# Kernel tuning notes

Hardware: AMD Instinct MI355X
Metric: run time of the kernel (lower is better)

Reference implementation:

```python
import jax, jax.numpy as jnp
import numpy as np

N = 100000          # nodes
E = 1600000         # edges (before self-loops)
F_IN = 128          # dataset.num_node_features
HID = 32            # hidden_channels
HEADS = 4
NUM_CLASSES = 40
NEG_SLOPE = 0.2     # PyG GATConv default


def setup_inputs() -> dict:
    key = jax.random.key(0)
    ks = jax.random.split(key, 16)
    x = jax.random.normal(ks[0], (N, F_IN), dtype=jnp.float32)
    edge_index = jax.random.randint(ks[1], (2, E), 0, N, dtype=jnp.int64)

    def glorot(k, shape):
        lim = float(np.sqrt(6.0 / (shape[0] + shape[-1])))
        return jax.random.uniform(k, shape, jnp.float32, -lim, lim)

    # layer 0: F_IN -> HID, heads=HEADS, concat
    W0 = glorot(ks[2], (F_IN, HEADS * HID))
    as0 = glorot(ks[3], (HEADS, HID))
    ad0 = glorot(ks[4], (HEADS, HID))
    b0 = jnp.zeros((HEADS * HID,), jnp.float32)
    # layer 1: HEADS*HID -> HID, heads=HEADS, concat
    W1 = glorot(ks[5], (HEADS * HID, HEADS * HID))
    as1 = glorot(ks[6], (HEADS, HID))
    ad1 = glorot(ks[7], (HEADS, HID))
    b1 = jnp.zeros((HEADS * HID,), jnp.float32)
    # layer 2: HEADS*HID -> HID, heads=1, no concat
    W2 = glorot(ks[8], (HEADS * HID, HID))
    as2 = glorot(ks[9], (1, HID))
    ad2 = glorot(ks[10], (1, HID))
    b2 = jnp.zeros((HID,), jnp.float32)
    # final linear HID -> NUM_CLASSES
    lin_w = glorot(ks[11], (HID, NUM_CLASSES))
    lin_b = jnp.zeros((NUM_CLASSES,), jnp.float32)
    return dict(x=x, edge_index=edge_index, W0=W0, as0=as0, ad0=ad0, b0=b0,
                W1=W1, as1=as1, ad1=ad1, b1=b1,
                W2=W2, as2=as2, ad2=ad2, b2=b2, lin_w=lin_w, lin_b=lin_b)


def gat_conv(x, src, dst, W, a_src, a_dst, b, heads, out_ch, concat):
    n = x.shape[0]
    h = (x @ W).reshape(n, heads, out_ch)               # [N,H,C]
    alpha_s = (h * a_src).sum(-1)                        # [N,H]
    alpha_d = (h * a_dst).sum(-1)                        # [N,H]
    e = jax.nn.leaky_relu(alpha_s[src] + alpha_d[dst], NEG_SLOPE)  # [E,H]
    m = jax.ops.segment_max(e, dst, num_segments=n)      # segment softmax over in-edges
    e = jnp.exp(e - m[dst])
    denom = jax.ops.segment_sum(e, dst, num_segments=n)
    alpha = e / (denom[dst] + 1e-16)                     # [E,H]
    out = jax.ops.segment_sum(h[src] * alpha[:, :, None], dst, num_segments=n)  # [N,H,C]
    out = out.reshape(n, heads * out_ch) if concat else out.mean(axis=1)
    return out + b


def reference(x, edge_index, W0, as0, ad0, b0, W1, as1, ad1, b1,
              W2, as2, ad2, b2, lin_w, lin_b):
    n = x.shape[0]
    loop = jnp.arange(n, dtype=edge_index.dtype)
    src = jnp.concatenate([edge_index[0], loop])   # PyG GATConv adds self-loops
    dst = jnp.concatenate([edge_index[1], loop])
    x = jax.nn.relu(gat_conv(x, src, dst, W0, as0, ad0, b0, HEADS, HID, True))
    x = jax.nn.relu(gat_conv(x, src, dst, W1, as1, ad1, b1, HEADS, HID, True))
    x = jax.nn.relu(gat_conv(x, src, dst, W2, as2, ad2, b2, 1, HID, False))
    return x @ lin_w + lin_b
```

## Files before the change

kernel.cpp:

```cpp
#include <hip/hip_runtime.h>
#include <hip/hip_bf16.h>
#include <hip/hip_fp16.h>
#include <math.h>


#define NEG_SLOPE 0.2f


__global__ void zero1_kernel(int* __restrict__ a, int n) {
    int i = blockIdx.x * blockDim.x + threadIdx.x;
    if (i < n) a[i] = 0;
}

__global__ void count_rank_kernel(const int* __restrict__ ei, int eraw, int n,
                                  int* __restrict__ deg, int* __restrict__ rank) {
    int i = blockIdx.x * blockDim.x + threadIdx.x;
    int etot = eraw + n;
    if (i >= etot) return;
    int dst = (i < eraw) ? ei[eraw + i] : (i - eraw);
    rank[i] = atomicAdd(&deg[dst], 1);
}

__global__ __launch_bounds__(1024)
void scan_local_kernel(const int* __restrict__ deg, int* __restrict__ rowptr,
                       int* __restrict__ bsum, int n) {
    __shared__ int buf[1024];
    int tid = threadIdx.x;
    int i = blockIdx.x * 1024 + tid;
    int v = (i < n) ? deg[i] : 0;
    buf[tid] = v;
    __syncthreads();
    for (int off = 1; off < 1024; off <<= 1) {
        int t = (tid >= off) ? buf[tid - off] : 0;
        __syncthreads();
        buf[tid] += t;
        __syncthreads();
    }
    if (i < n) rowptr[i] = buf[tid] - v;
    if (tid == 1023) bsum[blockIdx.x] = buf[1023];
}

__global__ __launch_bounds__(128)
void scan_sums_kernel(const int* __restrict__ bsum, int* __restrict__ boffs, int nb) {
    __shared__ int buf[128];
    int tid = threadIdx.x;
    int v = (tid < nb) ? bsum[tid] : 0;
    buf[tid] = v;
    __syncthreads();
    for (int off = 1; off < 128; off <<= 1) {
        int t = (tid >= off) ? buf[tid - off] : 0;
        __syncthreads();
        buf[tid] += t;
        __syncthreads();
    }
    if (tid < nb) boffs[tid] = buf[tid] - v;
}

__global__ void scan_add_kernel(int* __restrict__ rowptr, const int* __restrict__ boffs,
                                int n, int etot) {
    int i = blockIdx.x * blockDim.x + threadIdx.x;
    if (i < n) rowptr[i] += boffs[i >> 10];
    if (i == 0) rowptr[n] = etot;
}

__global__ void scatter2_kernel(const int* __restrict__ ei, const int* __restrict__ rank,
                                int eraw, int n, const int* __restrict__ rowptr,
                                int* __restrict__ csr_src) {
    int i = blockIdx.x * blockDim.x + threadIdx.x;
    int etot = eraw + n;
    if (i >= etot) return;
    int src, dst;
    if (i < eraw) { src = ei[i]; dst = ei[eraw + i]; }
    else          { src = i - eraw; dst = src; }
    csr_src[rowptr[dst] + rank[i]] = src;
}


struct h4pack { __half2 a, b; };

__global__ __launch_bounds__(256)
void gemm_rt_f32in_kernel(const float* __restrict__ X, const float* __restrict__ W,
                          __half* __restrict__ H, int n) {
    __shared__ float xsT[128][36];
    int t = threadIdx.x;
    int base = blockIdx.x * 32;
    {
        int r  = t >> 3;
        int k0 = (t & 7) << 4;
        const float4* xp = (const float4*)(X + (size_t)(base + r) * 128 + k0);
        float4 a = xp[0], b = xp[1], c = xp[2], d = xp[3];
        xsT[k0 +  0][r] = a.x; xsT[k0 +  1][r] = a.y; xsT[k0 +  2][r] = a.z; xsT[k0 +  3][r] = a.w;
        xsT[k0 +  4][r] = b.x; xsT[k0 +  5][r] = b.y; xsT[k0 +  6][r] = b.z; xsT[k0 +  7][r] = b.w;
        xsT[k0 +  8][r] = c.x; xsT[k0 +  9][r] = c.y; xsT[k0 + 10][r] = c.z; xsT[k0 + 11][r] = c.w;
        xsT[k0 + 12][r] = d.x; xsT[k0 + 13][r] = d.y; xsT[k0 + 14][r] = d.z; xsT[k0 + 15][r] = d.w;
    }
    __syncthreads();

    int tx = t & 31;
    int ty = t >> 5;
    float4 acc0 = make_float4(0.f, 0.f, 0.f, 0.f);
    float4 acc1 = acc0, acc2 = acc0, acc3 = acc0;
    const float4* W4 = (const float4*)W;

#pragma unroll 4
    for (int k = 0; k < 128; k++) {
        float4 w  = W4[k * 32 + tx];
        float4 xv = *(const float4*)(&xsT[k][ty << 2]);
        acc0.x += xv.x * w.x; acc0.y += xv.x * w.y; acc0.z += xv.x * w.z; acc0.w += xv.x * w.w;
        acc1.x += xv.y * w.x; acc1.y += xv.y * w.y; acc1.z += xv.y * w.z; acc1.w += xv.y * w.w;
        acc2.x += xv.z * w.x; acc2.y += xv.z * w.y; acc2.z += xv.z * w.z; acc2.w += xv.z * w.w;
        acc3.x += xv.w * w.x; acc3.y += xv.w * w.y; acc3.z += xv.w * w.z; acc3.w += xv.w * w.w;
    }

    size_t row0 = (size_t)(base + (ty << 2));
    h4pack* hp = (h4pack*)(H + row0 * 128) + tx;
    h4pack p;
    p.a = __floats2half2_rn(acc0.x, acc0.y); p.b = __floats2half2_rn(acc0.z, acc0.w);
    hp[0]  = p;
    p.a = __floats2half2_rn(acc1.x, acc1.y); p.b = __floats2half2_rn(acc1.z, acc1.w);
    hp[32] = p;
    p.a = __floats2half2_rn(acc2.x, acc2.y); p.b = __floats2half2_rn(acc2.z, acc2.w);
    hp[64] = p;
    p.a = __floats2half2_rn(acc3.x, acc3.y); p.b = __floats2half2_rn(acc3.z, acc3.w);
    hp[96] = p;
}

__global__ __launch_bounds__(256)
void gemm_rt_f16in_kernel(const __half* __restrict__ X, const float* __restrict__ W,
                          __half* __restrict__ H, int n) {
    __shared__ float xsT[128][36];
    int t = threadIdx.x;
    int base = blockIdx.x * 32;
    {
        int r  = t >> 3;
        int k0 = (t & 7) << 4;
        const uint4* xp = (const uint4*)(X + (size_t)(base + r) * 128 + k0);
        uint4 a = xp[0], b = xp[1];
        float2 f;
        f = __half22float2(*(const __half2*)&a.x); xsT[k0 +  0][r] = f.x; xsT[k0 +  1][r] = f.y;
        f = __half22float2(*(const __half2*)&a.y); xsT[k0 +  2][r] = f.x; xsT[k0 +  3][r] = f.y;
        f = __half22float2(*(const __half2*)&a.z); xsT[k0 +  4][r] = f.x; xsT[k0 +  5][r] = f.y;
        f = __half22float2(*(const __half2*)&a.w); xsT[k0 +  6][r] = f.x; xsT[k0 +  7][r] = f.y;
        f = __half22float2(*(const __half2*)&b.x); xsT[k0 +  8][r] = f.x; xsT[k0 +  9][r] = f.y;
        f = __half22float2(*(const __half2*)&b.y); xsT[k0 + 10][r] = f.x; xsT[k0 + 11][r] = f.y;
        f = __half22float2(*(const __half2*)&b.z); xsT[k0 + 12][r] = f.x; xsT[k0 + 13][r] = f.y;
        f = __half22float2(*(const __half2*)&b.w); xsT[k0 + 14][r] = f.x; xsT[k0 + 15][r] = f.y;
    }
    __syncthreads();

    int tx = t & 31;
    int ty = t >> 5;
    float4 acc0 = make_float4(0.f, 0.f, 0.f, 0.f);
    float4 acc1 = acc0, acc2 = acc0, acc3 = acc0;
    const float4* W4 = (const float4*)W;

#pragma unroll 4
    for (int k = 0; k < 128; k++) {
        float4 w  = W4[k * 32 + tx];
        float4 xv = *(const float4*)(&xsT[k][ty << 2]);
        acc0.x += xv.x * w.x; acc0.y += xv.x * w.y; acc0.z += xv.x * w.z; acc0.w += xv.x * w.w;
        acc1.x += xv.y * w.x; acc1.y += xv.y * w.y; acc1.z += xv.y * w.z; acc1.w += xv.y * w.w;
        acc2.x += xv.z * w.x; acc2.y += xv.z * w.y; acc2.z += xv.z * w.z; acc2.w += xv.z * w.w;
        acc3.x += xv.w * w.x; acc3.y += xv.w * w.y; acc3.z += xv.w * w.z; acc3.w += xv.w * w.w;
    }

    size_t row0 = (size_t)(base + (ty << 2));
    h4pack* hp = (h4pack*)(H + row0 * 128) + tx;
    h4pack p;
    p.a = __floats2half2_rn(acc0.x, acc0.y); p.b = __floats2half2_rn(acc0.z, acc0.w);
    hp[0]  = p;
    p.a = __floats2half2_rn(acc1.x, acc1.y); p.b = __floats2half2_rn(acc1.z, acc1.w);
    hp[32] = p;
    p.a = __floats2half2_rn(acc2.x, acc2.y); p.b = __floats2half2_rn(acc2.z, acc2.w);
    hp[64] = p;
    p.a = __floats2half2_rn(acc3.x, acc3.y); p.b = __floats2half2_rn(acc3.z, acc3.w);
    hp[96] = p;
}


__global__ __launch_bounds__(128)
void gemm_l2_f16_kernel(const __half* __restrict__ X, const float* __restrict__ W,
                        __half* __restrict__ H, int n) {
    __shared__ float xs[8][129];
    int base = blockIdx.x * 8;
    int tid = threadIdx.x;
#pragma unroll
    for (int it = 0; it < 4; it++) {
        int i = tid + it * 128;
        int r = i >> 6, c2 = i & 63;
        int row = base + r;
        __half2 v = (row < n) ? ((const __half2*)(X + (size_t)row * 128))[c2]
                              : __floats2half2_rn(0.f, 0.f);
        float2 f = __half22float2(v);
        xs[r][c2 * 2] = f.x; xs[r][c2 * 2 + 1] = f.y;
    }
    __syncthreads();
    int col  = tid & 31;
    int rsub = tid >> 5;
    float acc0 = 0.f, acc1 = 0.f;
    for (int k = 0; k < 128; k++) {
        float w = W[k * 32 + col];
        acc0 += xs[rsub][k] * w;
        acc1 += xs[rsub + 4][k] * w;
    }
    int row0 = base + rsub;
    if (row0 < n)     H[(size_t)row0 * 32 + col]       = __float2half(acc0);
    if (row0 + 4 < n) H[(size_t)(row0 + 4) * 32 + col] = __float2half(acc1);
}


__global__ void attn_coef_f16_kernel(const __half* __restrict__ H,
                                     const float* __restrict__ a_s,
                                     const float* __restrict__ a_d,
                                     float* __restrict__ as_out,
                                     float* __restrict__ ad_out, int n) {
    int i = blockIdx.x * blockDim.x + threadIdx.x;
    if (i >= n * 4) return;
    int node = i >> 2, h = i & 3;
    const __half2* hp = (const __half2*)(H + (size_t)node * 128 + h * 32);
    float s = 0.f, d = 0.f;
#pragma unroll
    for (int c2 = 0; c2 < 16; c2++) {
        float2 v = __half22float2(hp[c2]);
        s += v.x * a_s[h * 32 + c2 * 2] + v.y * a_s[h * 32 + c2 * 2 + 1];
        d += v.x * a_d[h * 32 + c2 * 2] + v.y * a_d[h * 32 + c2 * 2 + 1];
    }
    as_out[i] = s;
    ad_out[i] = d;
}

__global__ void attn_coef_l2_f16_kernel(const __half* __restrict__ H,
                                        const float* __restrict__ a_s,
                                        const float* __restrict__ a_d,
                                        float* __restrict__ as_out,
                                        float* __restrict__ ad_out, int n) {
    int i = blockIdx.x * blockDim.x + threadIdx.x;
    if (i >= n) return;
    const __half2* hp = (const __half2*)(H + (size_t)i * 32);
    float s = 0.f, d = 0.f;
#pragma unroll
    for (int c2 = 0; c2 < 16; c2++) {
        float2 v = __half22float2(hp[c2]);
        s += v.x * a_s[2 * c2] + v.y * a_s[2 * c2 + 1];
        d += v.x * a_d[2 * c2] + v.y * a_d[2 * c2 + 1];
    }
    as_out[i] = s;
    ad_out[i] = d;
}


__global__ __launch_bounds__(256)
void gat_fused_f16_kernel(const __half* __restrict__ Hm,
                          const float* __restrict__ as_,
                          const float* __restrict__ ad_,
                          const int* __restrict__ rowptr,
                          const int* __restrict__ csr,
                          const float* __restrict__ bias,
                          __half* __restrict__ out, int n) {
    constexpr int GS = 32;
    int t = threadIdx.x;
    int node = blockIdx.x * 8 + (t >> 5);
    if (node >= n) return;
    int tl = t & 31;
    int h  = tl >> 3;
    int k8 = tl & 7;
    const uint2* H8 = (const uint2*)Hm;
    int e0 = rowptr[node], e1 = rowptr[node + 1];
    float ad_d = ad_[(size_t)node * 4 + h];

    int  ce  = e0 + k8;
    bool vA  = ce < e1;
    int  idxA = vA ? csr[ce] : 0;
    float asA = vA ? as_[(size_t)idxA * 4 + h] : 0.f;

    float m = -INFINITY, l = 0.f;
    float4 acc = make_float4(0.f, 0.f, 0.f, 0.f);

    for (int eb = e0; eb < e1; eb += 8) {
        uint2 u[8];
#pragma unroll
        for (int j = 0; j < 8; j++) {
            int src = __shfl(idxA, j, 8);
            u[j] = H8[(size_t)src * GS + tl];
        }

        int  ne  = eb + 8 + k8;
        bool vB  = ne < e1;
        int  idxB = vB ? csr[ne] : 0;
        float asB = vB ? as_[(size_t)idxB * 4 + h] : 0.f;

        float el = asA + ad_d;
        el = (el > 0.f) ? el : NEG_SLOPE * el;
        el = vA ? el : -INFINITY;

        float cm = el;
        cm = fmaxf(cm, __shfl_xor(cm, 1, 8));
        cm = fmaxf(cm, __shfl_xor(cm, 2, 8));
        cm = fmaxf(cm, __shfl_xor(cm, 4, 8));
        float m_new = fmaxf(m, cm);
        float scale = __expf(m - m_new);
        float p = vA ? __expf(el - m_new) : 0.f;

        float ps = p;
        ps += __shfl_xor(ps, 1, 8);
        ps += __shfl_xor(ps, 2, 8);
        ps += __shfl_xor(ps, 4, 8);
        l = l * scale + ps;
        acc.x *= scale; acc.y *= scale; acc.z *= scale; acc.w *= scale;
        m = m_new;

#pragma unroll
        for (int j = 0; j < 8; j++) {
            float pj  = __shfl(p, j, 8);
            float2 f01 = __half22float2(*(const __half2*)&u[j].x);
            float2 f23 = __half22float2(*(const __half2*)&u[j].y);
            acc.x += pj * f01.x; acc.y += pj * f01.y;
            acc.z += pj * f23.x; acc.w += pj * f23.y;
        }
        idxA = idxB; asA = asB; vA = vB;
    }

    float li = 1.f / (l + 1e-16f);
    float4 b4 = ((const float4*)bias)[tl];
    float4 o;
    o.x = fmaxf(acc.x * li + b4.x, 0.f);
    o.y = fmaxf(acc.y * li + b4.y, 0.f);
    o.z = fmaxf(acc.z * li + b4.z, 0.f);
    o.w = fmaxf(acc.w * li + b4.w, 0.f);
    h4pack po;
    po.a = __floats2half2_rn(o.x, o.y);
    po.b = __floats2half2_rn(o.z, o.w);
    ((h4pack*)out)[(size_t)node * 32 + tl] = po;
}


__global__ __launch_bounds__(256)
void gat_fused_l2_kernel(const __half* __restrict__ Hm,
                         const float* __restrict__ as_,
                         const float* __restrict__ ad_,
                         const int* __restrict__ rowptr,
                         const int* __restrict__ csr,
                         const float* __restrict__ bias,
                         const float* __restrict__ lw,
                         const float* __restrict__ lb,
                         float* __restrict__ out, int n) {
    int t = threadIdx.x;
    int node = blockIdx.x * 32 + (t >> 3);
    if (node >= n) return;
    int tl = t & 7;
    const uint2* H8 = (const uint2*)Hm;
    int e0 = rowptr[node], e1 = rowptr[node + 1];
    float ad_d = ad_[node];

    int  ce  = e0 + tl;
    bool vA  = ce < e1;
    int  idxA = vA ? csr[ce] : 0;
    float asA = vA ? as_[idxA] : 0.f;

    float m = -INFINITY, l = 0.f;
    float4 acc = make_float4(0.f, 0.f, 0.f, 0.f);

    for (int eb = e0; eb < e1; eb += 8) {
        uint2 u[8];
#pragma unroll
        for (int j = 0; j < 8; j++) {
            int src = __shfl(idxA, j, 8);
            u[j] = H8[(size_t)src * 8 + tl];
        }

        int  ne  = eb + 8 + tl;
        bool vB  = ne < e1;
        int  idxB = vB ? csr[ne] : 0;
        float asB = vB ? as_[idxB] : 0.f;

        float el = asA + ad_d;
        el = (el > 0.f) ? el : NEG_SLOPE * el;
        el = vA ? el : -INFINITY;

        float cm = el;
        cm = fmaxf(cm, __shfl_xor(cm, 1, 8));
        cm = fmaxf(cm, __shfl_xor(cm, 2, 8));
        cm = fmaxf(cm, __shfl_xor(cm, 4, 8));
        float m_new = fmaxf(m, cm);
        float scale = __expf(m - m_new);
        float p = vA ? __expf(el - m_new) : 0.f;

        float ps = p;
        ps += __shfl_xor(ps, 1, 8);
        ps += __shfl_xor(ps, 2, 8);
        ps += __shfl_xor(ps, 4, 8);
        l = l * scale + ps;
        acc.x *= scale; acc.y *= scale; acc.z *= scale; acc.w *= scale;
        m = m_new;

#pragma unroll
        for (int j = 0; j < 8; j++) {
            float pj  = __shfl(p, j, 8);
            float2 f01 = __half22float2(*(const __half2*)&u[j].x);
            float2 f23 = __half22float2(*(const __half2*)&u[j].y);
            acc.x += pj * f01.x; acc.y += pj * f01.y;
            acc.z += pj * f23.x; acc.w += pj * f23.y;
        }
        idxA = idxB; asA = asB; vA = vB;
    }

    float li = 1.f / (l + 1e-16f);
    float4 b4 = ((const float4*)bias)[tl];
    float4 o;
    o.x = fmaxf(acc.x * li + b4.x, 0.f);
    o.y = fmaxf(acc.y * li + b4.y, 0.f);
    o.z = fmaxf(acc.z * li + b4.z, 0.f);
    o.w = fmaxf(acc.w * li + b4.w, 0.f);

    float fin0 = lb[tl];
    float fin1 = lb[tl + 8];
    float fin2 = lb[tl + 16];
    float fin3 = lb[tl + 24];
    float fin4 = lb[tl + 32];
#pragma unroll
    for (int j = 0; j < 8; j++) {
        float vx = __shfl(o.x, j, 8);
        float vy = __shfl(o.y, j, 8);
        float vz = __shfl(o.z, j, 8);
        float vw = __shfl(o.w, j, 8);
        const float* l0 = lw + (size_t)(4 * j) * 40;
#pragma unroll
        for (int c = 0; c < 5; c++) {
            int cls = tl + 8 * c;
            float v = vx * l0[cls] + vy * l0[40 + cls] + vz * l0[80 + cls] + vw * l0[120 + cls];
            if (c == 0) fin0 += v;
            else if (c == 1) fin1 += v;
            else if (c == 2) fin2 += v;
            else if (c == 3) fin3 += v;
            else fin4 += v;
        }
    }
    float* op = out + (size_t)node * 40;
    op[tl]      = fin0;
    op[tl + 8]  = fin1;
    op[tl + 16] = fin2;
    op[tl + 24] = fin3;
    op[tl + 32] = fin4;
}


extern "C" void kernel_launch(void* const* d_in, const int* in_sizes, int n_in,
                              void* d_out, int out_size, void* d_ws, size_t ws_size,
                              hipStream_t stream) {
    const float* x   = (const float*)d_in[0];
    const int*   ei  = (const int*)d_in[1];
    const float* W0  = (const float*)d_in[2];
    const float* as0 = (const float*)d_in[3];
    const float* ad0 = (const float*)d_in[4];
    const float* b0  = (const float*)d_in[5];
    const float* W1  = (const float*)d_in[6];
    const float* as1 = (const float*)d_in[7];
    const float* ad1 = (const float*)d_in[8];
    const float* b1  = (const float*)d_in[9];
    const float* W2  = (const float*)d_in[10];
    const float* as2 = (const float*)d_in[11];
    const float* ad2 = (const float*)d_in[12];
    const float* b2  = (const float*)d_in[13];
    const float* lw  = (const float*)d_in[14];
    const float* lb  = (const float*)d_in[15];
    float* out = (float*)d_out;

    const int n    = in_sizes[0] / 128;
    const int eraw = in_sizes[1] / 2;
    const int etot = eraw + n;
    const int nb   = (n + 1023) / 1024;

    char* wsp = (char*)d_ws;
    size_t off = 0;
    auto alloc = [&](size_t bytes) -> void* {
        void* p = wsp + off;
        off += (bytes + 255) & ~(size_t)255;
        return p;
    };
    __half* h16    = (__half*)alloc((size_t)n * 128 * 2);
    __half* buf16  = (__half*)alloc((size_t)n * 128 * 2);
    __half* h2     = (__half*)alloc((size_t)n * 32 * 2);
    float*  asb    = (float*)alloc((size_t)n * 4 * 4);
    float*  adb    = (float*)alloc((size_t)n * 4 * 4);
    int*    deg    = (int*)alloc((size_t)n * 4);
    int*    rank   = (int*)alloc((size_t)etot * 4);
    int*    rowptr = (int*)alloc((size_t)(n + 1) * 4);
    int*    csr    = (int*)alloc((size_t)etot * 4);
    int*    bsum   = (int*)alloc((size_t)nb * 4);
    int*    boffs  = (int*)alloc((size_t)nb * 4);

    zero1_kernel<<<(n + 255) / 256, 256, 0, stream>>>(deg, n);
    count_rank_kernel<<<(etot + 255) / 256, 256, 0, stream>>>(ei, eraw, n, deg, rank);
    scan_local_kernel<<<nb, 1024, 0, stream>>>(deg, rowptr, bsum, n);
    scan_sums_kernel<<<1, 128, 0, stream>>>(bsum, boffs, nb);
    scan_add_kernel<<<(n + 255) / 256, 256, 0, stream>>>(rowptr, boffs, n, etot);
    scatter2_kernel<<<(etot + 255) / 256, 256, 0, stream>>>(ei, rank, eraw, n, rowptr, csr);

    gemm_rt_f32in_kernel<<<n / 32, 256, 0, stream>>>(x, W0, h16, n);
    attn_coef_f16_kernel<<<(n * 4 + 255) / 256, 256, 0, stream>>>(h16, as0, ad0, asb, adb, n);
    gat_fused_f16_kernel<<<(n + 7) / 8, 256, 0, stream>>>(h16, asb, adb, rowptr, csr, b0, buf16, n);

    gemm_rt_f16in_kernel<<<n / 32, 256, 0, stream>>>(buf16, W1, h16, n);
    attn_coef_f16_kernel<<<(n * 4 + 255) / 256, 256, 0, stream>>>(h16, as1, ad1, asb, adb, n);
    gat_fused_f16_kernel<<<(n + 7) / 8, 256, 0, stream>>>(h16, asb, adb, rowptr, csr, b1, buf16, n);

    gemm_l2_f16_kernel<<<(n + 7) / 8, 128, 0, stream>>>(buf16, W2, h2, n);
    attn_coef_l2_f16_kernel<<<(n + 255) / 256, 256, 0, stream>>>(h2, as2, ad2, asb, adb, n);
    gat_fused_l2_kernel<<<(n + 31) / 32, 256, 0, stream>>>(h2, asb, adb, rowptr, csr, b2, lw, lb, out, n);
}
```

Before: 571.1 us.

## Replace FP32 scalar GEMMs for layers 0 and 1 with MFMA f16 matrix cores

The two 128x128 feature-transform GEMMs move from LDS-tiled FP32 FMA loops to MFMA 16x16x32 f16 instructions. Each wave computes 16 rows by 128 columns, and W is read from a pre-transposed f16 copy produced by a small new kernel. The goal is to cut ALU time in these GEMMs. In exchange, the inputs are rounded to f16 before multiplying, which lowers precision, and the output stores become scattered 2-byte writes.

```diff
diff --git a/kernel.cpp b/kernel.cpp
--- a/kernel.cpp
+++ b/kernel.cpp
@@ -5,6 +5,9 @@
 
 
 #define NEG_SLOPE 0.2f
+
+typedef __attribute__((ext_vector_type(8))) _Float16 f16x8;
+typedef __attribute__((ext_vector_type(4))) float    f32x4;
 
 
 __global__ void zero1_kernel(int* __restrict__ a, int n) {
@@ -76,105 +79,89 @@
 }
 
 
-struct h4pack { __half2 a, b; };
+__global__ void wt_f16_kernel(const float* __restrict__ W, __half* __restrict__ Wt) {
+    int i = blockIdx.x * blockDim.x + threadIdx.x;
+    int k = i >> 7, c = i & 127;
+    Wt[c * 128 + k] = __float2half(W[i]);
+}
+
 
 __global__ __launch_bounds__(256)
-void gemm_rt_f32in_kernel(const float* __restrict__ X, const float* __restrict__ W,
-                          __half* __restrict__ H, int n) {
-    __shared__ float xsT[128][36];
+void gemm_mfma_f32in_kernel(const float* __restrict__ X, const __half* __restrict__ Wt,
+                            __half* __restrict__ H, int n) {
     int t = threadIdx.x;
-    int base = blockIdx.x * 32;
-    {
-        int r  = t >> 3;
-        int k0 = (t & 7) << 4;
-        const float4* xp = (const float4*)(X + (size_t)(base + r) * 128 + k0);
-        float4 a = xp[0], b = xp[1], c = xp[2], d = xp[3];
-        xsT[k0 +  0][r] = a.x; xsT[k0 +  1][r] = a.y; xsT[k0 +  2][r] = a.z; xsT[k0 +  3][r] = a.w;
-        xsT[k0 +  4][r] = b.x; xsT[k0 +  5][r] = b.y; xsT[k0 +  6][r] = b.z; xsT[k0 +  7][r] = b.w;
-        xsT[k0 +  8][r] = c.x; xsT[k0 +  9][r] = c.y; xsT[k0 + 10][r] = c.z; xsT[k0 + 11][r] = c.w;
-        xsT[k0 + 12][r] = d.x; xsT[k0 + 13][r] = d.y; xsT[k0 + 14][r] = d.z; xsT[k0 + 15][r] = d.w;
-    }
-    __syncthreads();
-
-    int tx = t & 31;
-    int ty = t >> 5;
-    float4 acc0 = make_float4(0.f, 0.f, 0.f, 0.f);
-    float4 acc1 = acc0, acc2 = acc0, acc3 = acc0;
-    const float4* W4 = (const float4*)W;
-
-#pragma unroll 4
-    for (int k = 0; k < 128; k++) {
-        float4 w  = W4[k * 32 + tx];
-        float4 xv = *(const float4*)(&xsT[k][ty << 2]);
-        acc0.x += xv.x * w.x; acc0.y += xv.x * w.y; acc0.z += xv.x * w.z; acc0.w += xv.x * w.w;
-        acc1.x += xv.y * w.x; acc1.y += xv.y * w.y; acc1.z += xv.y * w.z; acc1.w += xv.y * w.w;
-        acc2.x += xv.z * w.x; acc2.y += xv.z * w.y; acc2.z += xv.z * w.z; acc2.w += xv.z * w.w;
-        acc3.x += xv.w * w.x; acc3.y += xv.w * w.y; acc3.z += xv.w * w.z; acc3.w += xv.w * w.w;
-    }
-
-    size_t row0 = (size_t)(base + (ty << 2));
-    h4pack* hp = (h4pack*)(H + row0 * 128) + tx;
-    h4pack p;
-    p.a = __floats2half2_rn(acc0.x, acc0.y); p.b = __floats2half2_rn(acc0.z, acc0.w);
-    hp[0]  = p;
-    p.a = __floats2half2_rn(acc1.x, acc1.y); p.b = __floats2half2_rn(acc1.z, acc1.w);
-    hp[32] = p;
-    p.a = __floats2half2_rn(acc2.x, acc2.y); p.b = __floats2half2_rn(acc2.z, acc2.w);
-    hp[64] = p;
-    p.a = __floats2half2_rn(acc3.x, acc3.y); p.b = __floats2half2_rn(acc3.z, acc3.w);
-    hp[96] = p;
+    int wave = t >> 6, lane = t & 63;
+    int l15 = lane & 15;
+    int kg  = lane >> 4;
+    int base = blockIdx.x * 64 + wave * 16;
+    int row  = base + l15;
+    int rowc = (row < n) ? row : 0;
+
+    f32x4 acc[8];
+#pragma unroll
+    for (int i = 0; i < 8; i++) acc[i] = (f32x4){0.f, 0.f, 0.f, 0.f};
+
+    const float* xp = X + (size_t)rowc * 128 + kg * 8;
+#pragma unroll
+    for (int ks = 0; ks < 4; ks++) {
+        float4 x0 = *(const float4*)(xp + ks * 32);
+        float4 x1 = *(const float4*)(xp + ks * 32 + 4);
+        f16x8 a;
+        a[0] = (_Float16)x0.x; a[1] = (_Float16)x0.y; a[2] = (_Float16)x0.z; a[3] = (_Float16)x0.w;
+        a[4] = (_Float16)x1.x; a[5] = (_Float16)x1.y; a[6] = (_Float16)x1.z; a[7] = (_Float16)x1.w;
+#pragma unroll
+        for (int ct = 0; ct < 8; ct++) {
+            f16x8 b = *(const f16x8*)(Wt + (size_t)(ct * 16 + l15) * 128 + ks * 32 + kg * 8);
+            acc[ct] = __builtin_amdgcn_mfma_f32_16x16x32_f16(a, b, acc[ct], 0, 0, 0);
+        }
+    }
+
+#pragma unroll
+    for (int ct = 0; ct < 8; ct++) {
+#pragma unroll
+        for (int r = 0; r < 4; r++) {
+            int orow = base + kg * 4 + r;
+            if (orow < n)
+                H[(size_t)orow * 128 + ct * 16 + l15] = __float2half(acc[ct][r]);
+        }
+    }
 }
 
 __global__ __launch_bounds__(256)
-void gemm_rt_f16in_kernel(const __half* __restrict__ X, const float* __restrict__ W,
-                          __half* __restrict__ H, int n) {
-    __shared__ float xsT[128][36];
+void gemm_mfma_f16in_kernel(const __half* __restrict__ X, const __half* __restrict__ Wt,
+                            __half* __restrict__ H, int n) {
     int t = threadIdx.x;
-    int base = blockIdx.x * 32;
-    {
-        int r  = t >> 3;
-        int k0 = (t & 7) << 4;
-        const uint4* xp = (const uint4*)(X + (size_t)(base + r) * 128 + k0);
-        uint4 a = xp[0], b = xp[1];
-        float2 f;
-        f = __half22float2(*(const __half2*)&a.x); xsT[k0 +  0][r] = f.x; xsT[k0 +  1][r] = f.y;
-        f = __half22float2(*(const __half2*)&a.y); xsT[k0 +  2][r] = f.x; xsT[k0 +  3][r] = f.y;
-        f = __half22float2(*(const __half2*)&a.z); xsT[k0 +  4][r] = f.x; xsT[k0 +  5][r] = f.y;
-        f = __half22float2(*(const __half2*)&a.w); xsT[k0 +  6][r] = f.x; xsT[k0 +  7][r] = f.y;
-        f = __half22float2(*(const __half2*)&b.x); xsT[k0 +  8][r] = f.x; xsT[k0 +  9][r] = f.y;
-        f = __half22float2(*(const __half2*)&b.y); xsT[k0 + 10][r] = f.x; xsT[k0 + 11][r] = f.y;
-        f = __half22float2(*(const __half2*)&b.z); xsT[k0 + 12][r] = f.x; xsT[k0 + 13][r] = f.y;
-        f = __half22float2(*(const __half2*)&b.w); xsT[k0 + 14][r] = f.x; xsT[k0 + 15][r] = f.y;
-    }
-    __syncthreads();
-
-    int tx = t & 31;
-    int ty = t >> 5;
-    float4 acc0 = make_float4(0.f, 0.f, 0.f, 0.f);
-    float4 acc1 = acc0, acc2 = acc0, acc3 = acc0;
-    const float4* W4 = (const float4*)W;
-
-#pragma unroll 4
-    for (int k = 0; k < 128; k++) {
-        float4 w  = W4[k * 32 + tx];
-        float4 xv = *(const float4*)(&xsT[k][ty << 2]);
-        acc0.x += xv.x * w.x; acc0.y += xv.x * w.y; acc0.z += xv.x * w.z; acc0.w += xv.x * w.w;
-        acc1.x += xv.y * w.x; acc1.y += xv.y * w.y; acc1.z += xv.y * w.z; acc1.w += xv.y * w.w;
-        acc2.x += xv.z * w.x; acc2.y += xv.z * w.y; acc2.z += xv.z * w.z; acc2.w += xv.z * w.w;
-        acc3.x += xv.w * w.x; acc3.y += xv.w * w.y; acc3.z += xv.w * w.z; acc3.w += xv.w * w.w;
-    }
-
-    size_t row0 = (size_t)(base + (ty << 2));
-    h4pack* hp = (h4pack*)(H + row0 * 128) + tx;
-    h4pack p;
-    p.a = __floats2half2_rn(acc0.x, acc0.y); p.b = __floats2half2_rn(acc0.z, acc0.w);
-    hp[0]  = p;
-    p.a = __floats2half2_rn(acc1.x, acc1.y); p.b = __floats2half2_rn(acc1.z, acc1.w);
-    hp[32] = p;
-    p.a = __floats2half2_rn(acc2.x, acc2.y); p.b = __floats2half2_rn(acc2.z, acc2.w);
-    hp[64] = p;
-    p.a = __floats2half2_rn(acc3.x, acc3.y); p.b = __floats2half2_rn(acc3.z, acc3.w);
-    hp[96] = p;
+    int wave = t >> 6, lane = t & 63;
+    int l15 = lane & 15;
+    int kg  = lane >> 4;
+    int base = blockIdx.x * 64 + wave * 16;
+    int row  = base + l15;
+    int rowc = (row < n) ? row : 0;
+
+    f32x4 acc[8];
+#pragma unroll
+    for (int i = 0; i < 8; i++) acc[i] = (f32x4){0.f, 0.f, 0.f, 0.f};
+
+    const __half* xp = X + (size_t)rowc * 128 + kg * 8;
+#pragma unroll
+    for (int ks = 0; ks < 4; ks++) {
+        f16x8 a = *(const f16x8*)(xp + ks * 32);
+#pragma unroll
+        for (int ct = 0; ct < 8; ct++) {
+            f16x8 b = *(const f16x8*)(Wt + (size_t)(ct * 16 + l15) * 128 + ks * 32 + kg * 8);
+            acc[ct] = __builtin_amdgcn_mfma_f32_16x16x32_f16(a, b, acc[ct], 0, 0, 0);
+        }
+    }
+
+#pragma unroll
+    for (int ct = 0; ct < 8; ct++) {
+#pragma unroll
+        for (int r = 0; r < 4; r++) {
+            int orow = base + kg * 4 + r;
+            if (orow < n)
+                H[(size_t)orow * 128 + ct * 16 + l15] = __float2half(acc[ct][r]);
+        }
+    }
 }
 
 
@@ -248,6 +235,8 @@
     ad_out[i] = d;
 }
 
+
+struct h4pack { __half2 a, b; };
 
 __global__ __launch_bounds__(256)
 void gat_fused_f16_kernel(const __half* __restrict__ Hm,
@@ -480,6 +469,8 @@
     __half* h16    = (__half*)alloc((size_t)n * 128 * 2);
     __half* buf16  = (__half*)alloc((size_t)n * 128 * 2);
     __half* h2     = (__half*)alloc((size_t)n * 32 * 2);
+    __half* Wt0    = (__half*)alloc((size_t)128 * 128 * 2);
+    __half* Wt1    = (__half*)alloc((size_t)128 * 128 * 2);
     float*  asb    = (float*)alloc((size_t)n * 4 * 4);
     float*  adb    = (float*)alloc((size_t)n * 4 * 4);
     int*    deg    = (int*)alloc((size_t)n * 4);
@@ -491,16 +482,18 @@
 
     zero1_kernel<<<(n + 255) / 256, 256, 0, stream>>>(deg, n);
     count_rank_kernel<<<(etot + 255) / 256, 256, 0, stream>>>(ei, eraw, n, deg, rank);
+    wt_f16_kernel<<<64, 256, 0, stream>>>(W0, Wt0);
+    wt_f16_kernel<<<64, 256, 0, stream>>>(W1, Wt1);
     scan_local_kernel<<<nb, 1024, 0, stream>>>(deg, rowptr, bsum, n);
     scan_sums_kernel<<<1, 128, 0, stream>>>(bsum, boffs, nb);
     scan_add_kernel<<<(n + 255) / 256, 256, 0, stream>>>(rowptr, boffs, n, etot);
     scatter2_kernel<<<(etot + 255) / 256, 256, 0, stream>>>(ei, rank, eraw, n, rowptr, csr);
 
-    gemm_rt_f32in_kernel<<<n / 32, 256, 0, stream>>>(x, W0, h16, n);
+    gemm_mfma_f32in_kernel<<<(n + 63) / 64, 256, 0, stream>>>(x, Wt0, h16, n);
     attn_coef_f16_kernel<<<(n * 4 + 255) / 256, 256, 0, stream>>>(h16, as0, ad0, asb, adb, n);
     gat_fused_f16_kernel<<<(n + 7) / 8, 256, 0, stream>>>(h16, asb, adb, rowptr, csr, b0, buf16, n);
 
-    gemm_rt_f16in_kernel<<<n / 32, 256, 0, stream>>>(buf16, W1, h16, n);
+    gemm_mfma_f16in_kernel<<<(n + 63) / 64, 256, 0, stream>>>(buf16, Wt1, h16, n);
     attn_coef_f16_kernel<<<(n * 4 + 255) / 256, 256, 0, stream>>>(h16, as1, ad1, asb, adb, n);
     gat_fused_f16_kernel<<<(n + 7) / 8, 256, 0, stream>>>(h16, asb, adb, rowptr, csr, b1, buf16, n);
 
```

After: 528.8 us. -7.4%, faster.
